# Kernel tuning notes

Hardware: AMD Instinct MI355X
Metric: run time of the kernel (lower is better)

The kernel has to match this reference:

```python
import jax, jax.numpy as jnp
import numpy as np
from jax import lax

NUM_CLASSES = 9
N_BOXES = 6
LEVELS = [(32, 256), (16, 128), (8, 64), (4, 32), (2, 16), (1, 8)]
BATCH = 8


def _conv(x, w, b):
    # x: [N,C,H,W], w: [O,I,3,3] -> same-padded stride-1 conv (padding=1)
    y = lax.conv_general_dilated(x, w, window_strides=(1, 1), padding='SAME',
                                 dimension_numbers=('NCHW', 'OIHW', 'NCHW'))
    return y + b[None, :, None, None]


def _head(x, ws, bs, w_out, b_out):
    for i in range(4):
        x = jax.nn.relu(_conv(x, ws[i], bs[i]))
    return _conv(x, w_out, b_out)


def setup_inputs() -> dict:
    key = jax.random.key(0)
    ks = jax.random.split(key, 12)
    inp = {}
    for i, (h, w) in enumerate(LEVELS):
        inp[f'feat{i}'] = jax.random.normal(ks[i], (BATCH, 256, h, w), dtype=jnp.float32)
    std = 0.01  # matches _init_improved_weights: normal(0, 0.01), bias=0
    inp['reg_w'] = jax.random.normal(ks[6], (4, 256, 256, 3, 3), dtype=jnp.float32) * std
    inp['reg_b'] = jnp.zeros((4, 256), dtype=jnp.float32)
    inp['reg_w_out'] = jax.random.normal(ks[7], (N_BOXES * 4, 256, 3, 3), dtype=jnp.float32) * std
    inp['reg_b_out'] = jnp.zeros((N_BOXES * 4,), dtype=jnp.float32)
    inp['cls_w'] = jax.random.normal(ks[8], (4, 256, 256, 3, 3), dtype=jnp.float32) * std
    inp['cls_b'] = jnp.zeros((4, 256), dtype=jnp.float32)
    inp['cls_w_out'] = jax.random.normal(ks[9], (N_BOXES * NUM_CLASSES, 256, 3, 3), dtype=jnp.float32) * std
    inp['cls_b_out'] = jnp.zeros((N_BOXES * NUM_CLASSES,), dtype=jnp.float32)
    return inp


def reference(feat0, feat1, feat2, feat3, feat4, feat5,
              reg_w, reg_b, reg_w_out, reg_b_out,
              cls_w, cls_b, cls_w_out, cls_b_out):
    features = [feat0, feat1, feat2, feat3, feat4, feat5]
    locations, confidences = [], []
    for x in features:
        n = x.shape[0]
        bbox_delta = _head(x, reg_w, reg_b, reg_w_out, reg_b_out).reshape(n, 4, -1)
        bbox_conf = _head(x, cls_w, cls_b, cls_w_out, cls_b_out).reshape(n, NUM_CLASSES, -1)
        locations.append(bbox_delta)
        confidences.append(bbox_conf)
    bbox_delta = jnp.concatenate(locations, axis=2)   # [N, 4, total_anchors]
    confs = jnp.concatenate(confidences, axis=2)      # [N, num_classes, total_anchors]
    return (bbox_delta, confs)
```

## Files before the change

kernel.cpp:

```cpp
#include <hip/hip_runtime.h>
#include <hip/hip_bf16.h>


typedef float  f32x4 __attribute__((ext_vector_type(4)));
typedef int    i32x4 __attribute__((ext_vector_type(4)));
typedef int    i32x2 __attribute__((ext_vector_type(2)));
typedef __bf16 bfrag __attribute__((ext_vector_type(8)));
typedef __bf16 bf4   __attribute__((ext_vector_type(4)));

struct LevelD {
  int H, W, logW, logHW, P, HW, act_off, aoff, blk_start, pos_start;
};
struct Desc  { LevelD lv[6]; };
struct FPtrs { const float* f[6]; };

#define ACT_ELEMS  24735744
#define WREG_OFF   0
#define WCLS_OFF   2359296
#define WREGO_OFF  4718592
#define WCLSO_OFF  4773888
#define ACT0_OFF   4898304
#define ACT1_OFF   29634048
#define ACT2_OFF   54369792
#define WS_ELEMS   54369792ull
#define TOTAL_ANCH 65520
#define CLS_BASE   2096640
#define NPAD_JOBS  9264

__device__ __forceinline__ void glds16(const __bf16* g, __bf16* l) {
  __builtin_amdgcn_global_load_lds(
      (const __attribute__((address_space(1))) void*)g,
      (__attribute__((address_space(3))) void*)l, 16, 0, 0);
}

__device__ __forceinline__ int xcd_swz(int b, int nwg) {
  int xcd = b & 7;
  int q = nwg >> 3, r = nwg & 7;
  int base = (xcd < r) ? xcd * (q + 1) : r * (q + 1) + (xcd - r) * q;
  return base + (b >> 3);
}

__global__ __launch_bounds__(256) void padzero_k(__bf16* __restrict__ act, int nbuf)
{
  static const int kHh[6]   = {32, 16, 8, 4, 2, 1};
  static const int kWw[6]   = {256, 128, 64, 32, 16, 8};
  static const int kOff[6]  = {0, 17965056, 22757376, 24109056, 24526848, 24674304};
  static const int kPer[6]  = {580, 292, 148, 76, 40, 22};
  static const int kCum[7]  = {0, 4640, 6976, 8160, 8768, 9088, 9264};
  int job  = blockIdx.x * 4 + (threadIdx.x >> 6);
  int lane = threadIdx.x & 63;
  int nb = job / NPAD_JOBS;
  if (nb >= nbuf) return;
  int e8 = job - nb * NPAD_JOBS;
  int li = 0;
  #pragma unroll
  for (int i = 1; i < 6; ++i) li = (e8 >= kCum[i]) ? i : li;
  int r = e8 - kCum[li];
  int per = kPer[li];
  int n = r / per;
  int e = r - n * per;
  int H = kHh[li], W = kWw[li], Wp = W + 2;
  int y, x;
  if (e < 2 * Wp) {
    y = (e < Wp) ? 0 : (H + 1);
    x = (e < Wp) ? e : (e - Wp);
  } else {
    int e2 = e - 2 * Wp;
    x = (e2 < H) ? 0 : (W + 1);
    y = 1 + ((e2 < H) ? e2 : (e2 - H));
  }
  size_t base = (size_t)nb * ACT_ELEMS + kOff[li]
              + ((size_t)((n * (H + 2) + y) * Wp + x) << 8) + (lane << 2);
  i32x2 z = {0, 0};
  *(i32x2*)(act + base) = z;
}

__global__ __launch_bounds__(256) void prep_k(const float* __restrict__ w,
                                              __bf16* __restrict__ o, int total)
{
  for (int i = blockIdx.x * 256 + threadIdx.x; i < total; i += gridDim.x * 256) {
    int co = i / 2304;
    int r  = i - co * 2304;
    int t  = r >> 8;
    int ci = r & 255;
    o[i] = (__bf16)w[((co << 8) + ci) * 9 + t];
  }
}

__global__ __launch_bounds__(256) void convert_k(FPtrs fp, __bf16* __restrict__ act, Desc d)
{
  __shared__ __bf16 T[16 * 264];
  int b  = blockIdx.x;
  int p0 = b << 4;
  int li = 0;
  #pragma unroll
  for (int i = 1; i < 6; ++i) li = (p0 >= d.lv[i].pos_start) ? i : li;
  LevelD L = d.lv[li];
  int lp  = b * 16 - L.pos_start;
  int tid = threadIdx.x;
  int pl = tid & 15;
  int p  = lp + pl;
  int n  = p >> L.logHW;
  int y  = (p >> L.logW) & (L.H - 1);
  int x  = p & (L.W - 1);
  const float* src = fp.f[li];
  size_t base = (size_t)n * ((size_t)L.HW << 8) + (size_t)y * L.W + x;
  int c0 = tid >> 4;
  #pragma unroll
  for (int it = 0; it < 16; ++it) {
    int c = c0 + (it << 4);
    T[pl * 264 + c] = (__bf16)src[base + (size_t)c * L.HW];
  }
  __syncthreads();
  int p2 = tid >> 4;
  int cc = (tid & 15) << 4;
  int pg = lp + p2;
  int n2 = pg >> L.logHW;
  int y2 = (pg >> L.logW) & (L.H - 1);
  int x2 = pg & (L.W - 1);
  __bf16* dst = act + L.act_off +
      ((size_t)((n2 * (L.H + 2) + y2 + 1) * (L.W + 2) + x2 + 1) << 8) + cc;
  i32x4 v0 = *(const i32x4*)&T[p2 * 264 + cc];
  i32x4 v1 = *(const i32x4*)&T[p2 * 264 + cc + 8];
  *(i32x4*)dst       = v0;
  *(i32x4*)(dst + 8) = v1;
}

__global__ __launch_bounds__(512, 2)
void conv_mid_k(const __bf16* __restrict__ inb, __bf16* __restrict__ outb,
                const __bf16* __restrict__ wT, const float* __restrict__ bias,
                Desc d)
{
  __shared__ __bf16 Asm[3][8192];
  __shared__ __bf16 Bsm[3][6144];
  int b  = xcd_swz(blockIdx.x, 459);
  int li = 0;
  #pragma unroll
  for (int i = 1; i < 6; ++i) li = (b >= d.lv[i].blk_start) ? i : li;
  LevelD L = d.lv[li];
  int p0 = (b - L.blk_start) * 192;
  int tid  = threadIdx.x;
  int lane = tid & 63;
  int wv   = tid >> 6;
  int wm = wv >> 2, wn = wv & 3;
  int fr = lane & 15, fg = lane >> 4;
  int Wp = L.W + 2;

  const __bf16* gA[2];
  int ldsA[2];
  #pragma unroll
  for (int r = 0; r < 2; ++r) {
    int row = (r << 7) + (wv << 4) + (lane >> 2);
    int sw  = (lane & 3) ^ ((row >> 1) & 3);
    gA[r] = wT + row * 2304 + (sw << 3);
    ldsA[r] = ((r << 7) + (wv << 4)) << 5;
  }
  bool bact = lane < 48;
  const __bf16* gB[2];
  int ldsB[2];
  #pragma unroll
  for (int r = 0; r < 2; ++r) {
    int row = r * 96 + wv * 12 + (lane >> 2);
    int sw  = (lane & 3) ^ ((row >> 1) & 3);
    int p  = p0 + row;
    int pc = (p < L.P) ? p : 0;
    int n  = pc >> L.logHW;
    int y  = (pc >> L.logW) & (L.H - 1);
    int x  = pc & (L.W - 1);
    gB[r] = inb + L.act_off + (((n * (L.H + 2) + y) * Wp + x) << 8) + (sw << 3);
    ldsB[r] = (r * 96 + wv * 12) << 5;
  }

  int offA[8], offB[3];
  #pragma unroll
  for (int mf = 0; mf < 8; ++mf) {
    int row = (wm << 7) + (mf << 4) + fr;
    offA[mf] = (row << 5) + ((fg ^ ((fr >> 1) & 3)) << 3);
  }
  #pragma unroll
  for (int nf = 0; nf < 3; ++nf) {
    int row = wn * 48 + (nf << 4) + fr;
    offB[nf] = (row << 5) + ((fg ^ ((fr >> 1) & 3)) << 3);
  }

  auto stageA = [&](int kt, int buf) {
    int ko = ((kt >> 3) << 8) + ((kt & 7) << 5);
    glds16(gA[0] + ko, &Asm[buf][ldsA[0]]);
    glds16(gA[1] + ko, &Asm[buf][ldsA[1]]);
  };
  auto stageB = [&](int kt, int buf) {
    int t  = kt >> 3;
    int ky = (t >= 6) ? 2 : (t >= 3 ? 1 : 0);
    int kx = t - ky * 3;
    int kb = ((ky * Wp + kx) << 8) + ((kt & 7) << 5);
    if (bact) {
      glds16(gB[0] + kb, &Bsm[buf][ldsB[0]]);
      glds16(gB[1] + kb, &Bsm[buf][ldsB[1]]);
    }
  };

  f32x4 acc[8][3] = {};

  stageA(0, 0); stageB(0, 0);
  stageA(1, 1); stageB(1, 1);

  int cur = 0;
  #pragma unroll 1
  for (int kt = 0; kt < 72; ++kt) {
    int sbuf = cur + 2; if (sbuf >= 3) sbuf -= 3;
    bool st = (kt < 70);

    if (kt == 71) { asm volatile("s_waitcnt vmcnt(0)" ::: "memory"); }
    else          { asm volatile("s_waitcnt vmcnt(4)" ::: "memory"); }
    __builtin_amdgcn_s_barrier();
    asm volatile("" ::: "memory");
    bfrag bf3[3], a0, a1, a2, a3;
    #pragma unroll
    for (int nf = 0; nf < 3; ++nf) bf3[nf] = *(const bfrag*)&Bsm[cur][offB[nf]];
    a0 = *(const bfrag*)&Asm[cur][offA[0]];
    a1 = *(const bfrag*)&Asm[cur][offA[1]];
    a2 = *(const bfrag*)&Asm[cur][offA[2]];
    a3 = *(const bfrag*)&Asm[cur][offA[3]];
    if (st) stageA(kt + 2, sbuf);
    asm volatile("s_waitcnt lgkmcnt(0)" ::: "memory");
    __builtin_amdgcn_sched_barrier(0);
    __builtin_amdgcn_s_setprio(1);
    #pragma unroll
    for (int nf = 0; nf < 3; ++nf) {
      acc[0][nf] = __builtin_amdgcn_mfma_f32_16x16x32_bf16(a0, bf3[nf], acc[0][nf], 0, 0, 0);
      acc[1][nf] = __builtin_amdgcn_mfma_f32_16x16x32_bf16(a1, bf3[nf], acc[1][nf], 0, 0, 0);
      acc[2][nf] = __builtin_amdgcn_mfma_f32_16x16x32_bf16(a2, bf3[nf], acc[2][nf], 0, 0, 0);
      acc[3][nf] = __builtin_amdgcn_mfma_f32_16x16x32_bf16(a3, bf3[nf], acc[3][nf], 0, 0, 0);
    }
    __builtin_amdgcn_s_setprio(0);

    __builtin_amdgcn_s_barrier();
    asm volatile("" ::: "memory");
    a0 = *(const bfrag*)&Asm[cur][offA[4]];
    a1 = *(const bfrag*)&Asm[cur][offA[5]];
    a2 = *(const bfrag*)&Asm[cur][offA[6]];
    a3 = *(const bfrag*)&Asm[cur][offA[7]];
    if (st) stageB(kt + 2, sbuf);
    asm volatile("s_waitcnt lgkmcnt(0)" ::: "memory");
    __builtin_amdgcn_sched_barrier(0);
    __builtin_amdgcn_s_setprio(1);
    #pragma unroll
    for (int nf = 0; nf < 3; ++nf) {
      acc[4][nf] = __builtin_amdgcn_mfma_f32_16x16x32_bf16(a0, bf3[nf], acc[4][nf], 0, 0, 0);
      acc[5][nf] = __builtin_amdgcn_mfma_f32_16x16x32_bf16(a1, bf3[nf], acc[5][nf], 0, 0, 0);
      acc[6][nf] = __builtin_amdgcn_mfma_f32_16x16x32_bf16(a2, bf3[nf], acc[6][nf], 0, 0, 0);
      acc[7][nf] = __builtin_amdgcn_mfma_f32_16x16x32_bf16(a3, bf3[nf], acc[7][nf], 0, 0, 0);
    }
    __builtin_amdgcn_s_setprio(0);

    ++cur; if (cur == 3) cur = 0;
  }

  #pragma unroll
  for (int nf = 0; nf < 3; ++nf) {
    int pp = p0 + wn * 48 + (nf << 4) + fr;
    if (pp >= L.P) continue;
    int n2 = pp >> L.logHW;
    int y2 = (pp >> L.logW) & (L.H - 1);
    int x2 = pp & (L.W - 1);
    __bf16* ob = outb + L.act_off + (((n2 * (L.H + 2) + y2 + 1) * Wp + x2 + 1) << 8);
    #pragma unroll
    for (int mf = 0; mf < 8; ++mf) {
      int cob = (wm << 7) + (mf << 4) + (fg << 2);
      f32x4 bb = *(const f32x4*)(bias + cob);
      f32x4 v  = acc[mf][nf];
      bf4 ov;
      #pragma unroll
      for (int j = 0; j < 4; ++j) ov[j] = (__bf16)fmaxf(v[j] + bb[j], 0.0f);
      *(bf4*)(ob + cob) = ov;
    }
  }
}

__global__ __launch_bounds__(256, 3)
void conv_out_k(const __bf16* __restrict__ inb, const __bf16* __restrict__ wT,
                const float* __restrict__ biasO, float* __restrict__ dout,
                Desc d, int Cout, int isCls)
{
  __shared__ __bf16 Asm[2][64 * 32];
  __shared__ __bf16 Bsm[2][128 * 32];
  int b  = xcd_swz(blockIdx.x, 683);
  int li = 0;
  #pragma unroll
  for (int i = 1; i < 6; ++i) li = (b >= d.lv[i].blk_start) ? i : li;
  LevelD L = d.lv[li];
  int p0 = (b - L.blk_start) << 7;
  int tid  = threadIdx.x;
  int lane = tid & 63;
  int wv   = tid >> 6;
  int fr = lane & 15, fg = lane >> 4;
  int Wp = L.W + 2;
  int nmf = (Cout + 15) >> 4;

  int rsub = lane >> 2;
  int slot = lane & 3;
  int sw   = slot ^ ((rsub >> 1) & 3);

  const __bf16* gA0;
  {
    int row = (wv << 4) + rsub;
    int co  = (row < Cout) ? row : 0;
    gA0 = wT + co * 2304 + (sw << 3);
  }
  const __bf16* gB[2];
  #pragma unroll
  for (int j = 0; j < 2; ++j) {
    int row = (j << 6) + (wv << 4) + rsub;
    int p  = p0 + row;
    int pc = (p < L.P) ? p : 0;
    int n = pc >> L.logHW, y = (pc >> L.logW) & (L.H - 1), x = pc & (L.W - 1);
    gB[j] = inb + L.act_off + (((n * (L.H + 2) + y) * Wp + x) << 8) + (sw << 3);
  }
  int dW = (wv << 4) << 5;

  int csw = ((fg ^ ((fr >> 1) & 3)) << 3);
  int offA[4], offB[2];
  #pragma unroll
  for (int mf = 0; mf < 4; ++mf)
    offA[mf] = (((mf << 4) + fr) << 5) + csw;
  #pragma unroll
  for (int nf = 0; nf < 2; ++nf)
    offB[nf] = (((wv << 5) + (nf << 4) + fr) << 5) + csw;

  auto stage = [&](int k, int bb) {
    int t  = k >> 3;
    int ky = (t >= 6) ? 2 : (t >= 3 ? 1 : 0);
    int kx = t - ky * 3;
    int ka = (t << 8) + ((k & 7) << 5);
    int kb = ((ky * Wp + kx) << 8) + ((k & 7) << 5);
    glds16(gA0 + ka, &Asm[bb][dW]);
    glds16(gB[0] + kb, &Bsm[bb][dW]);
    glds16(gB[1] + kb, &Bsm[bb][2048 + dW]);
  };

  f32x4 acc[4][2] = {};

  stage(0, 0);
  #pragma unroll 1
  for (int k = 0; k < 72; ++k) {
    int cur = k & 1;
    __syncthreads();
    if (k < 71) stage(k + 1, cur ^ 1);
    bfrag af[4], bfv[2];
    #pragma unroll
    for (int mf = 0; mf < 4; ++mf)
      if (mf < nmf) af[mf] = *(const bfrag*)&Asm[cur][offA[mf]];
    #pragma unroll
    for (int nf = 0; nf < 2; ++nf)
      bfv[nf] = *(const bfrag*)&Bsm[cur][offB[nf]];
    #pragma unroll
    for (int mf = 0; mf < 4; ++mf)
      if (mf < nmf)
        #pragma unroll
        for (int nf = 0; nf < 2; ++nf)
          acc[mf][nf] = __builtin_amdgcn_mfma_f32_16x16x32_bf16(
              af[mf], bfv[nf], acc[mf][nf], 0, 0, 0);
  }

  #pragma unroll
  for (int nf = 0; nf < 2; ++nf) {
    int pp = p0 + (wv << 5) + (nf << 4) + fr;
    if (pp >= L.P) continue;
    int n2 = pp >> L.logHW;
    int y2 = (pp >> L.logW) & (L.H - 1);
    int x2 = pp & (L.W - 1);
    int sp_off = L.aoff + y2 * L.W + x2;
    #pragma unroll
    for (int mf = 0; mf < 4; ++mf) {
      if (mf < nmf) {
        #pragma unroll
        for (int j = 0; j < 4; ++j) {
          int co = (mf << 4) + (fg << 2) + j;
          if (co < Cout) {
            float val = acc[mf][nf][j] + biasO[co];
            int g   = co / 6;
            int box = co - g * 6;
            size_t idx;
            if (isCls) idx = (size_t)CLS_BASE + ((size_t)n2 * 9 + g) * TOTAL_ANCH
                             + sp_off + box * L.HW;
            else       idx = ((size_t)n2 * 4 + g) * TOTAL_ANCH + sp_off + box * L.HW;
            dout[idx] = val;
          }
        }
      }
    }
  }
}

extern "C" void kernel_launch(void* const* d_in, const int* in_sizes, int n_in,
                              void* d_out, int out_size, void* d_ws, size_t ws_size,
                              hipStream_t stream) {
  if (ws_size < WS_ELEMS * 2) return;

  static const int kH[6]      = {32, 16, 8, 4, 2, 1};
  static const int kW[6]      = {256, 128, 64, 32, 16, 8};
  static const int kLogW[6]   = {8, 7, 6, 5, 4, 3};
  static const int kLogHW[6]  = {13, 11, 9, 7, 5, 3};
  static const int kActOff[6] = {0, 17965056, 22757376, 24109056, 24526848, 24674304};
  static const int kAoff[6]   = {0, 49152, 61440, 64512, 65280, 65472};
  static const int kBlkMid[6] = {0, 342, 428, 450, 456, 458};
  static const int kBlkOut[6] = {0, 512, 640, 672, 680, 682};
  static const int kPosSt[6]  = {0, 65536, 81920, 86016, 87040, 87296};

  FPtrs fp;
  for (int i = 0; i < 6; ++i) fp.f[i] = (const float*)d_in[i];
  const float* reg_w  = (const float*)d_in[6];
  const float* reg_b  = (const float*)d_in[7];
  const float* reg_wo = (const float*)d_in[8];
  const float* reg_bo = (const float*)d_in[9];
  const float* cls_w  = (const float*)d_in[10];
  const float* cls_b  = (const float*)d_in[11];
  const float* cls_wo = (const float*)d_in[12];
  const float* cls_bo = (const float*)d_in[13];
  __bf16* ws = (__bf16*)d_ws;

  Desc dmid, dout_d;
  for (int i = 0; i < 6; ++i) {
    LevelD L;
    L.H = kH[i]; L.W = kW[i]; L.logW = kLogW[i]; L.logHW = kLogHW[i];
    L.HW = kH[i] * kW[i]; L.P = 8 * L.HW;
    L.act_off = kActOff[i]; L.aoff = kAoff[i];
    L.pos_start = kPosSt[i];
    L.blk_start = kBlkMid[i];
    dmid.lv[i] = L;
    L.blk_start = kBlkOut[i];
    dout_d.lv[i] = L;
  }

  bool use3 = ws_size >= (size_t)(ACT0_OFF + 3ull * ACT_ELEMS) * 2ull;
  int nbuf = use3 ? 3 : 2;

  padzero_k<<<(NPAD_JOBS * nbuf + 3) / 4, 256, 0, stream>>>(ws + ACT0_OFF, nbuf);

  prep_k<<<256, 256, 0, stream>>>(reg_w,  ws + WREG_OFF,  1024 * 2304);
  prep_k<<<256, 256, 0, stream>>>(cls_w,  ws + WCLS_OFF,  1024 * 2304);
  prep_k<<<64,  256, 0, stream>>>(reg_wo, ws + WREGO_OFF, 24 * 2304);
  prep_k<<<64,  256, 0, stream>>>(cls_wo, ws + WCLSO_OFF, 54 * 2304);

  if (use3) {
    convert_k<<<5460, 256, 0, stream>>>(fp, ws + ACT2_OFF, dmid);
    for (int head = 0; head < 2; ++head) {
      const __bf16* wT = ws + (head ? WCLS_OFF : WREG_OFF);
      const float*  bb = head ? cls_b : reg_b;
      conv_mid_k<<<459, 512, 0, stream>>>(ws + ACT2_OFF, ws + ACT0_OFF, wT + 0 * 589824, bb + 0,   dmid);
      conv_mid_k<<<459, 512, 0, stream>>>(ws + ACT0_OFF, ws + ACT1_OFF, wT + 1 * 589824, bb + 256, dmid);
      conv_mid_k<<<459, 512, 0, stream>>>(ws + ACT1_OFF, ws + ACT0_OFF, wT + 2 * 589824, bb + 512, dmid);
      conv_mid_k<<<459, 512, 0, stream>>>(ws + ACT0_OFF, ws + ACT1_OFF, wT + 3 * 589824, bb + 768, dmid);
      conv_out_k<<<683, 256, 0, stream>>>(ws + ACT1_OFF,
          ws + (head ? WCLSO_OFF : WREGO_OFF), head ? cls_bo : reg_bo,
          (float*)d_out, dout_d, head ? 54 : 24, head);
    }
  } else {
    for (int head = 0; head < 2; ++head) {
      convert_k<<<5460, 256, 0, stream>>>(fp, ws + ACT0_OFF, dmid);
      const __bf16* wT = ws + (head ? WCLS_OFF : WREG_OFF);
      const float*  bb = head ? cls_b : reg_b;
      conv_mid_k<<<459, 512, 0, stream>>>(ws + ACT0_OFF, ws + ACT1_OFF, wT + 0 * 589824, bb + 0,   dmid);
      conv_mid_k<<<459, 512, 0, stream>>>(ws + ACT1_OFF, ws + ACT0_OFF, wT + 1 * 589824, bb + 256, dmid);
      conv_mid_k<<<459, 512, 0, stream>>>(ws + ACT0_OFF, ws + ACT1_OFF, wT + 2 * 589824, bb + 512, dmid);
      conv_mid_k<<<459, 512, 0, stream>>>(ws + ACT1_OFF, ws + ACT0_OFF, wT + 3 * 589824, bb + 768, dmid);
      conv_out_k<<<683, 256, 0, stream>>>(ws + ACT0_OFF,
          ws + (head ? WCLSO_OFF : WREGO_OFF), head ? cls_bo : reg_bo,
          (float*)d_out, dout_d, head ? 54 : 24, head);
    }
  }
}
```

Measured before the change: 1.208 ms.

## Switch mid conv kernel to 32x32x16 MFMA with 4x2 wave tiling

Replaces the 16x16x32 bf16 MFMA tiling of the mid-layer conv with 32x32x16 MFMAs. Waves are rearranged from 2x4 to 4x2, so each wave owns 64 output channels by 96 positions instead of 128 by 48. The inner k-step is merged into a single barrier phase that issues both A and B staging at once, dropping the second barrier and the explicit LDS waits. The epilogue is rewritten for the 32x32 accumulator layout. This aims at cutting sync overhead and LDS fragment reads per MFMA, but it changes the schedule and register pressure.

```diff
diff --git a/kernel.cpp b/kernel.cpp
--- a/kernel.cpp
+++ b/kernel.cpp
@@ -2,11 +2,12 @@
 #include <hip/hip_bf16.h>
 
 
-typedef float  f32x4 __attribute__((ext_vector_type(4)));
-typedef int    i32x4 __attribute__((ext_vector_type(4)));
-typedef int    i32x2 __attribute__((ext_vector_type(2)));
-typedef __bf16 bfrag __attribute__((ext_vector_type(8)));
-typedef __bf16 bf4   __attribute__((ext_vector_type(4)));
+typedef float  f32x4  __attribute__((ext_vector_type(4)));
+typedef float  f32x16 __attribute__((ext_vector_type(16)));
+typedef int    i32x4  __attribute__((ext_vector_type(4)));
+typedef int    i32x2  __attribute__((ext_vector_type(2)));
+typedef __bf16 bfrag  __attribute__((ext_vector_type(8)));
+typedef __bf16 bf4    __attribute__((ext_vector_type(4)));
 
 struct LevelD {
   int H, W, logW, logHW, P, HW, act_off, aoff, blk_start, pos_start;
@@ -142,8 +143,8 @@
   int tid  = threadIdx.x;
   int lane = tid & 63;
   int wv   = tid >> 6;
-  int wm = wv >> 2, wn = wv & 3;
-  int fr = lane & 15, fg = lane >> 4;
+  int wm = wv >> 1, wn = wv & 1;
+  int wl = lane & 31, lh = lane >> 5;
   int Wp = L.W + 2;
 
   const __bf16* gA[2];
@@ -171,16 +172,21 @@
     ldsB[r] = (r * 96 + wv * 12) << 5;
   }
 
-  int offA[8], offB[3];
-  #pragma unroll
-  for (int mf = 0; mf < 8; ++mf) {
-    int row = (wm << 7) + (mf << 4) + fr;
-    offA[mf] = (row << 5) + ((fg ^ ((fr >> 1) & 3)) << 3);
-  }
-  #pragma unroll
-  for (int nf = 0; nf < 3; ++nf) {
-    int row = wn * 48 + (nf << 4) + fr;
-    offB[nf] = (row << 5) + ((fg ^ ((fr >> 1) & 3)) << 3);
+  int fsw = (wl >> 1) & 3;
+  int offA[2][2], offB[3][2];
+  #pragma unroll
+  for (int ct = 0; ct < 2; ++ct) {
+    int row = (wm << 6) + (ct << 5) + wl;
+    #pragma unroll
+    for (int kk = 0; kk < 2; ++kk)
+      offA[ct][kk] = (row << 5) + (((((kk << 1) | lh)) ^ fsw) << 3);
+  }
+  #pragma unroll
+  for (int pt = 0; pt < 3; ++pt) {
+    int row = wn * 96 + (pt << 5) + wl;
+    #pragma unroll
+    for (int kk = 0; kk < 2; ++kk)
+      offB[pt][kk] = (row << 5) + (((((kk << 1) | lh)) ^ fsw) << 3);
   }
 
   auto stageA = [&](int kt, int buf) {
@@ -199,7 +205,7 @@
     }
   };
 
-  f32x4 acc[8][3] = {};
+  f32x16 acc[2][3] = {};
 
   stageA(0, 0); stageB(0, 0);
   stageA(1, 1); stageB(1, 1);
@@ -208,71 +214,62 @@
   #pragma unroll 1
   for (int kt = 0; kt < 72; ++kt) {
     int sbuf = cur + 2; if (sbuf >= 3) sbuf -= 3;
-    bool st = (kt < 70);
-
     if (kt == 71) { asm volatile("s_waitcnt vmcnt(0)" ::: "memory"); }
     else          { asm volatile("s_waitcnt vmcnt(4)" ::: "memory"); }
     __builtin_amdgcn_s_barrier();
     asm volatile("" ::: "memory");
-    bfrag bf3[3], a0, a1, a2, a3;
-    #pragma unroll
-    for (int nf = 0; nf < 3; ++nf) bf3[nf] = *(const bfrag*)&Bsm[cur][offB[nf]];
-    a0 = *(const bfrag*)&Asm[cur][offA[0]];
-    a1 = *(const bfrag*)&Asm[cur][offA[1]];
-    a2 = *(const bfrag*)&Asm[cur][offA[2]];
-    a3 = *(const bfrag*)&Asm[cur][offA[3]];
-    if (st) stageA(kt + 2, sbuf);
-    asm volatile("s_waitcnt lgkmcnt(0)" ::: "memory");
-    __builtin_amdgcn_sched_barrier(0);
+
+    bfrag a[2][2], bb[3][2];
+    #pragma unroll
+    for (int ct = 0; ct < 2; ++ct)
+      #pragma unroll
+      for (int kk = 0; kk < 2; ++kk)
+        a[ct][kk] = *(const bfrag*)&Asm[cur][offA[ct][kk]];
+    #pragma unroll
+    for (int pt = 0; pt < 3; ++pt)
+      #pragma unroll
+      for (int kk = 0; kk < 2; ++kk)
+        bb[pt][kk] = *(const bfrag*)&Bsm[cur][offB[pt][kk]];
+
+    if (kt < 70) { stageA(kt + 2, sbuf); stageB(kt + 2, sbuf); }
+
     __builtin_amdgcn_s_setprio(1);
     #pragma unroll
-    for (int nf = 0; nf < 3; ++nf) {
-      acc[0][nf] = __builtin_amdgcn_mfma_f32_16x16x32_bf16(a0, bf3[nf], acc[0][nf], 0, 0, 0);
-      acc[1][nf] = __builtin_amdgcn_mfma_f32_16x16x32_bf16(a1, bf3[nf], acc[1][nf], 0, 0, 0);
-      acc[2][nf] = __builtin_amdgcn_mfma_f32_16x16x32_bf16(a2, bf3[nf], acc[2][nf], 0, 0, 0);
-      acc[3][nf] = __builtin_amdgcn_mfma_f32_16x16x32_bf16(a3, bf3[nf], acc[3][nf], 0, 0, 0);
-    }
+    for (int ct = 0; ct < 2; ++ct)
+      #pragma unroll
+      for (int pt = 0; pt < 3; ++pt)
+        #pragma unroll
+        for (int kk = 0; kk < 2; ++kk)
+          acc[ct][pt] = __builtin_amdgcn_mfma_f32_32x32x16_bf16(
+              a[ct][kk], bb[pt][kk], acc[ct][pt], 0, 0, 0);
     __builtin_amdgcn_s_setprio(0);
 
-    __builtin_amdgcn_s_barrier();
-    asm volatile("" ::: "memory");
-    a0 = *(const bfrag*)&Asm[cur][offA[4]];
-    a1 = *(const bfrag*)&Asm[cur][offA[5]];
-    a2 = *(const bfrag*)&Asm[cur][offA[6]];
-    a3 = *(const bfrag*)&Asm[cur][offA[7]];
-    if (st) stageB(kt + 2, sbuf);
-    asm volatile("s_waitcnt lgkmcnt(0)" ::: "memory");
-    __builtin_amdgcn_sched_barrier(0);
-    __builtin_amdgcn_s_setprio(1);
-    #pragma unroll
-    for (int nf = 0; nf < 3; ++nf) {
-      acc[4][nf] = __builtin_amdgcn_mfma_f32_16x16x32_bf16(a0, bf3[nf], acc[4][nf], 0, 0, 0);
-      acc[5][nf] = __builtin_amdgcn_mfma_f32_16x16x32_bf16(a1, bf3[nf], acc[5][nf], 0, 0, 0);
-      acc[6][nf] = __builtin_amdgcn_mfma_f32_16x16x32_bf16(a2, bf3[nf], acc[6][nf], 0, 0, 0);
-      acc[7][nf] = __builtin_amdgcn_mfma_f32_16x16x32_bf16(a3, bf3[nf], acc[7][nf], 0, 0, 0);
-    }
-    __builtin_amdgcn_s_setprio(0);
-
     ++cur; if (cur == 3) cur = 0;
   }
 
   #pragma unroll
-  for (int nf = 0; nf < 3; ++nf) {
-    int pp = p0 + wn * 48 + (nf << 4) + fr;
-    if (pp >= L.P) continue;
-    int n2 = pp >> L.logHW;
-    int y2 = (pp >> L.logW) & (L.H - 1);
-    int x2 = pp & (L.W - 1);
-    __bf16* ob = outb + L.act_off + (((n2 * (L.H + 2) + y2 + 1) * Wp + x2 + 1) << 8);
-    #pragma unroll
-    for (int mf = 0; mf < 8; ++mf) {
-      int cob = (wm << 7) + (mf << 4) + (fg << 2);
-      f32x4 bb = *(const f32x4*)(bias + cob);
-      f32x4 v  = acc[mf][nf];
-      bf4 ov;
+  for (int ct = 0; ct < 2; ++ct) {
+    int cob = (wm << 6) + (ct << 5) + (lh << 2);
+    #pragma unroll
+    for (int pt = 0; pt < 3; ++pt) {
+      int pgrp = p0 + wn * 96 + (pt << 5);
+      if (pgrp >= L.P) continue;
+      int pos = pgrp + wl;
+      int n2 = pos >> L.logHW;
+      int y2 = (pos >> L.logW) & (L.H - 1);
+      int x2 = pos & (L.W - 1);
+      __bf16* ob = outb + L.act_off + (((n2 * (L.H + 2) + y2 + 1) * Wp + x2 + 1) << 8);
+      f32x16 v = acc[ct][pt];
       #pragma unroll
-      for (int j = 0; j < 4; ++j) ov[j] = (__bf16)fmaxf(v[j] + bb[j], 0.0f);
-      *(bf4*)(ob + cob) = ov;
+      for (int g = 0; g < 4; ++g) {
+        int co = cob + (g << 3);
+        f32x4 bb4 = *(const f32x4*)(bias + co);
+        bf4 ov;
+        #pragma unroll
+        for (int jj = 0; jj < 4; ++jj)
+          ov[jj] = (__bf16)fmaxf(v[(g << 2) + jj] + bb4[jj], 0.0f);
+        *(bf4*)(ob + co) = ov;
+      }
     }
   }
 }
```

Result: slower. 1.366 ms (+13.0%).
